# Optimization experiments

Measured on AMD Instinct MI355X. Metric: run time of the kernel, lower is better.

The kernel has to match this reference:

```python
import jax, jax.numpy as jnp
import numpy as np
from jax import lax
from jax.scipy.special import erf

EPS = 1e-5
B = 256

def _conv(x, w, stride):
    return lax.conv_general_dilated(x, w, (stride, stride), ((1, 1), (1, 1)),
                                    dimension_numbers=('NCHW', 'OIHW', 'NCHW'))

def lr_conv(x, alpha, betta, bias, stride):
    # Ternary weight distribution (LR-nets): p0 = P(w=0), p1 = P(w=1)
    p0 = jax.nn.sigmoid(alpha)
    p1 = (1.0 - p0) * jax.nn.sigmoid(betta)
    w_mean = 2.0 * p1 + p0 - 1.0          # E[w] = p1 - p_{-1}
    w_var = (1.0 - p0) - w_mean * w_mean  # Var[w] = E[w^2] - E[w]^2
    m = _conv(x, w_mean, stride) + bias[None, :, None, None]
    v = _conv(x * x, w_var, stride)
    return m, v

def sign_prob(m, v):
    # expected sign under CLT Gaussian: 2*Phi(m/sqrt(v)) - 1 = erf(m / sqrt(2 v))
    return erf(m / jnp.sqrt(2.0 * (v + EPS)))

def setup_inputs() -> dict:
    key = jax.random.key(0)
    ks = jax.random.split(key, 32)
    def n(k, shape, s=1.0):
        return jax.random.normal(k, shape, dtype=jnp.float32) * s
    inp = {}
    inp['x'] = n(ks[0], (B, 3, 32, 32))
    shapes = [(128, 3), (128, 128), (256, 128), (256, 256), (512, 256), (512, 512)]
    i = 1
    for li, (co, ci) in enumerate(shapes, start=1):
        inp['a%d' % li] = n(ks[i], (co, ci, 3, 3)); i += 1
        inp['b%d' % li] = n(ks[i], (co, ci, 3, 3)); i += 1
        inp['c%d' % li] = jnp.zeros((co,), jnp.float32)
    inp['bn_gamma'] = jnp.ones((512,), jnp.float32)
    inp['bn_beta'] = jnp.zeros((512,), jnp.float32)
    inp['fc1_w'] = n(ks[20], (1024, 8192), 0.01)
    inp['fc1_b'] = jnp.zeros((1024,), jnp.float32)
    inp['fc2_w'] = n(ks[21], (10, 1024), 0.03)
    inp['fc2_b'] = jnp.zeros((10,), jnp.float32)
    inp['noise6'] = n(ks[22], (B, 512, 4, 4))
    return inp

def reference(x, a1, b1, c1, a2, b2, c2, a3, b3, c3, a4, b4, c4, a5, b5, c5,
              a6, b6, c6, bn_gamma, bn_beta, fc1_w, fc1_b, fc2_w, fc2_b, noise6):
    h = x
    for (a, bt, c, s) in [(a1, b1, c1, 1), (a2, b2, c2, 2), (a3, b3, c3, 1),
                          (a4, b4, c4, 2), (a5, b5, c5, 1)]:
        m, v = lr_conv(h, a, bt, c, s)
        h = sign_prob(m, v)
    m, v = lr_conv(h, a6, b6, c6, 2)          # output_sample=True layer
    z = m + jnp.sqrt(v + EPS) * noise6        # reparameterized Gaussian sample
    mu = jnp.mean(z, axis=(0, 2, 3), keepdims=True)
    var = jnp.var(z, axis=(0, 2, 3), keepdims=True)
    z = bn_gamma[None, :, None, None] * (z - mu) / jnp.sqrt(var + EPS) + bn_beta[None, :, None, None]
    z = jax.nn.relu(z).reshape(z.shape[0], -1)  # [B, 8192]
    z = jax.nn.relu(z @ fc1_w.T + fc1_b)
    return z @ fc2_w.T + fc2_b
```

## Files before the change

kernel.cpp:

```cpp
#include <hip/hip_runtime.h>
#include <hip/hip_bf16.h>
#include <math.h>

#define EPS 1e-5f

typedef __hip_bfloat16 bf16;
typedef short s16x8 __attribute__((ext_vector_type(8)));
typedef float f32x4 __attribute__((ext_vector_type(4)));

constexpr int ilog2c(int v) { return v <= 1 ? 0 : 1 + ilog2c(v >> 1); }

__device__ __forceinline__ float ldin(const void* p, size_t i, int isbf) {
    return isbf ? __bfloat162float(((const bf16*)p)[i]) : ((const float*)p)[i];
}
__device__ __forceinline__ float b2f_bits(short s) {
    unsigned u = ((unsigned)(unsigned short)s) << 16;
    return __builtin_bit_cast(float, u);
}
__device__ __forceinline__ unsigned sqpk1(unsigned w) {
    float lo = __builtin_bit_cast(float, w << 16);
    float hi = __builtin_bit_cast(float, w & 0xffff0000u);
    lo *= lo; hi *= hi;
    unsigned ul = __builtin_bit_cast(unsigned, lo) + 0x8000u;
    unsigned uh = __builtin_bit_cast(unsigned, hi) + 0x8000u;
    return __builtin_amdgcn_perm(uh, ul, 0x07060302);
}
__device__ __forceinline__ uint4 sqpk4(uint4 u) {
    uint4 r;
    r.x = sqpk1(u.x); r.y = sqpk1(u.y); r.z = sqpk1(u.z); r.w = sqpk1(u.w);
    return r;
}

__device__ __forceinline__ void dma16(const void* g, void* l) {
    __builtin_amdgcn_global_load_lds(
        (const __attribute__((address_space(1))) void*)g,
        (__attribute__((address_space(3))) void*)l, 16, 0, 0);
}

__global__ __launch_bounds__(64) void detect_kernel(const void* __restrict__ x,
                                                    int* __restrict__ flags,
                                                    char* __restrict__ gA,
                                                    char* __restrict__ gB) {
    const unsigned* w = (const unsigned*)x;
    unsigned word = w[threadIdx.x];
    int e = (word >> 23) & 0xFF;
    bool ok = (word == 0u) || (e >= 0x70 && e <= 0x8E);
    unsigned long long m = __ballot(ok);
    if (threadIdx.x == 0) flags[0] = (__popcll(m) >= 32) ? 0 : 1;
    if (threadIdx.x < 16) ((uint4*)gA)[threadIdx.x] = (uint4){0, 0, 0, 0};
    else if (threadIdx.x < 32) ((uint4*)gB)[threadIdx.x - 16] = (uint4){0, 0, 0, 0};
}

__global__ __launch_bounds__(256) void prep_w_l1(
    const void* __restrict__ alpha, const void* __restrict__ betta,
    const int* __restrict__ flags, float* __restrict__ wmv, int n)
{
    int i = blockIdx.x * 256 + threadIdx.x;
    if (i >= n) return;
    int fl = flags[0];
    float a = ldin(alpha, i, fl), b = ldin(betta, i, fl);
    float p0 = 1.f / (1.f + expf(-a));
    float p1 = (1.f - p0) / (1.f + expf(-b));
    float m = 2.f * p1 + p0 - 1.f;
    wmv[i] = m;
    wmv[n + i] = (1.f - p0) - m * m;
}

__global__ __launch_bounds__(256) void prep_w_r(
    const void* __restrict__ alpha, const void* __restrict__ betta,
    const int* __restrict__ flags, bf16* __restrict__ wmr, bf16* __restrict__ wvr,
    int lc, int n)
{
    int o = blockIdx.x * 256 + threadIdx.x;
    if (o >= n) return;
    int fl = flags[0];
    int cotap = o >> lc;
    int ci = o & ((1 << lc) - 1);
    int co = cotap / 9;
    int tap = cotap - co * 9;
    int i = (((co << lc) + ci) * 9) + tap;
    float a = ldin(alpha, i, fl), b = ldin(betta, i, fl);
    float p0 = 1.f / (1.f + expf(-a));
    float p1 = (1.f - p0) / (1.f + expf(-b));
    float m = 2.f * p1 + p0 - 1.f;
    float v = (1.f - p0) - m * m;
    wmr[o] = __float2bfloat16(m);
    wvr[o] = __float2bfloat16(v);
}

__global__ __launch_bounds__(256) void permute_fc1(
    const void* __restrict__ w, const int* __restrict__ flags, bf16* __restrict__ wp)
{
    __shared__ float L[8192];
    const int fl = flags[0];
    int tid = threadIdx.x;
    int o = blockIdx.x;
    size_t srow = (size_t)o * 8192;
    for (int c = tid; c < 512; c += 256) {
        float v[16];
        if (fl) {
            const uint4* s = (const uint4*)((const bf16*)w + srow + c * 16);
            uint4 u0 = s[0], u1 = s[1];
            const unsigned short* h0 = (const unsigned short*)&u0;
            const unsigned short* h1 = (const unsigned short*)&u1;
#pragma unroll
            for (int j = 0; j < 8; j++) { v[j] = b2f_bits((short)h0[j]); v[8 + j] = b2f_bits((short)h1[j]); }
        } else {
            const float4* s = (const float4*)((const float*)w + srow + c * 16);
#pragma unroll
            for (int j = 0; j < 4; j++) {
                float4 t4 = s[j];
                v[j * 4 + 0] = t4.x; v[j * 4 + 1] = t4.y; v[j * 4 + 2] = t4.z; v[j * 4 + 3] = t4.w;
            }
        }
#pragma unroll
        for (int hw = 0; hw < 16; hw++) L[hw * 512 + c] = v[hw];
    }
    __syncthreads();
    for (int j = 0; j < 32; j++) {
        int idx = j * 256 + tid;
        wp[srow + idx] = __float2bfloat16(L[idx]);
    }
}

__global__ __launch_bounds__(256) void l1_conv(
    const void* __restrict__ x, const float* __restrict__ wmv,
    const void* __restrict__ bias, const int* __restrict__ flags,
    bf16* __restrict__ out)
{
    __shared__ float Xs[64][28];
    const int fl = flags[0];
    int tid = threadIdx.x;
    int pos0 = blockIdx.x * 64;
    int b = pos0 >> 10;
    for (int u = tid; u < 576; u += 256) {
        int p = u / 9, r = u - p * 9;
        int ci = r / 3, kh = r - ci * 3;
        int pos = pos0 + p;
        int oh = (pos >> 5) & 31, ow = pos & 31;
        int ih = oh - 1 + kh;
        bool okh = (unsigned)ih < 32u;
        size_t base = ((size_t)(b * 3 + ci) * 32 + ih) * 32;
#pragma unroll
        for (int kw = 0; kw < 3; kw++) {
            int iw = ow - 1 + kw;
            float v = (okh && (unsigned)iw < 32u) ? ldin(x, base + iw, fl) : 0.f;
            Xs[p][ci * 9 + kh * 3 + kw] = v;
        }
    }
    int c = tid & 127, pg = tid >> 7;
    float wm[27], wv[27];
#pragma unroll
    for (int k = 0; k < 27; k++) {
        wm[k] = wmv[c * 27 + k];
        wv[k] = wmv[3456 + c * 27 + k];
    }
    float bs = ldin(bias, c, fl);
    __syncthreads();
    for (int it = 0; it < 32; it++) {
        int p = it * 2 + pg;
        float aM = 0.f, aV = 0.f;
#pragma unroll
        for (int k = 0; k < 27; k++) {
            float xv = Xs[p][k];
            aM = fmaf(xv, wm[k], aM);
            aV = fmaf(xv * xv, wv[k], aV);
        }
        out[(size_t)(pos0 + p) * 128 + c] =
            __float2bfloat16(erff((aM + bs) * rsqrtf(2.f * (aV + EPS))));
    }
}

template<int CI, int CO, int H, int W, int S, int OH, int OW, int ACT, int COT>
__global__ __launch_bounds__(256, 3) void conv_gemm(
    const char* __restrict__ xreg,
    int zpoff,
    const bf16* __restrict__ wmr,
    const bf16* __restrict__ wvr,
    const void* __restrict__ bias, const void* __restrict__ noise,
    const int* __restrict__ flags, void* __restrict__ outp)
{
    constexpr int OHW = OH * OW;
    constexpr int KC = CI / 32;
    constexpr int NC = 9 * KC;
    constexpr int NW = COT / 16;
    constexpr int XB = 128 * 64;
    constexpr int WB = COT * 64;
    constexpr int BUFB = XB + 2 * WB;
    constexpr int LOHW = ilog2c(OHW), LOW = ilog2c(OW);
    static_assert((NC & 1) == 0 && COT == 64, "");

    __shared__ __align__(16) char smem[2 * BUFB];

    const int tid = threadIdx.x;
    const int lane = tid & 63, wv_ = tid >> 6;
    const int q = lane >> 4, l15 = lane & 15;
    const int pw = wv_ * 32;
    const int c0 = blockIdx.y * COT;
    const int bx128 = blockIdx.x * 128;

    const int sl   = (lane & 7) ^ (lane >> 3);
    const int row2 = 2 * (lane >> 3) + (sl >> 2);
    const int u16b = (sl & 3) * 16;

    int xb[4], ohS[4], owS[4];
#pragma unroll
    for (int kk = 0; kk < 4; kk++) {
        int P = bx128 + 16 * ((wv_ & 1) * 4 + kk) + row2;
        int bi = P >> LOHW;
        ohS[kk] = ((P >> LOW) & (OH - 1)) * S - 1;
        owS[kk] = (P & (OW - 1)) * S - 1;
        xb[kk] = bi * (H * W * CI * 2);
    }
    const char* wsb = (const char*)((wv_ == 3) ? wvr : wmr)
                      + (size_t)(c0 + row2) * (9 * CI * 2) + u16b;
    const int wdoff = XB + ((wv_ == 3) ? WB : 0);

    const int lA = (l15 >> 1) * 128 + (((((l15 & 1) << 2) | q) ^ (l15 >> 1)) << 4);
    const int abase = pw * 64 + lA;
    const int bbase = lA;

    f32x4 accM[2][4], accV[2][4];
#pragma unroll
    for (int i = 0; i < 2; i++)
#pragma unroll
        for (int j = 0; j < 4; j++) {
            accM[i][j] = (f32x4){0.f, 0.f, 0.f, 0.f};
            accV[i][j] = (f32x4){0.f, 0.f, 0.f, 0.f};
        }

    auto stage = [&](int t, int nb) {
        char* buf = smem + nb * BUFB;
        if (wv_ < 2) {
            const int tap = t / KC, kci = (t - tap * KC) * 64;
            const int kh = tap / 3, kw2 = tap - 3 * kh;
#pragma unroll
            for (int kk = 0; kk < 4; kk++) {
                int ih = ohS[kk] + kh, iw = owS[kk] + kw2;
                bool ok = ((unsigned)ih < (unsigned)H) && ((unsigned)iw < (unsigned)W);
                int off = xb[kk] + (ih * W + iw) * (CI * 2) + kci + u16b;
                off = ok ? off : zpoff;
                dma16(xreg + off, buf + ((wv_ & 1) * 4 + kk) * 1024);
            }
        } else {
            const char* s = wsb + t * 64;
            char* d = buf + wdoff;
#pragma unroll
            for (int k = 0; k < NW; k++)
                dma16(s + (size_t)k * (16 * 9 * CI * 2), d + k * 1024);
        }
    };

    auto compute = [&](int nb) {
        const char* buf = smem + nb * BUFB;
        s16x8 a[2], aq[2];
#pragma unroll
        for (int i = 0; i < 2; i++) {
            a[i] = *(const s16x8*)(buf + abase + i * 1024);
            uint4 uq = sqpk4(*(const uint4*)&a[i]);
            aq[i] = *(const s16x8*)&uq;
        }
#pragma unroll
        for (int j = 0; j < 4; j++) {
            s16x8 bm = *(const s16x8*)(buf + XB + bbase + j * 1024);
            s16x8 bv = *(const s16x8*)(buf + XB + WB + bbase + j * 1024);
#pragma unroll
            for (int i = 0; i < 2; i++) {
                accM[i][j] = __builtin_amdgcn_mfma_f32_16x16x32_bf16(a[i],  bm, accM[i][j], 0, 0, 0);
                accV[i][j] = __builtin_amdgcn_mfma_f32_16x16x32_bf16(aq[i], bv, accV[i][j], 0, 0, 0);
            }
        }
    };

#define BAR() asm volatile("s_waitcnt vmcnt(0) lgkmcnt(0)\n\ts_barrier" ::: "memory")

    stage(0, 0);
    for (int t = 0; t < NC; t += 2) {
        BAR();
        if (t + 1 < NC) stage(t + 1, 1);
        compute(0);
        BAR();
        if (t + 2 < NC) stage(t + 2, 0);
        compute(1);
    }
#undef BAR

    __syncthreads();
    const int fl = flags[0];
    if constexpr (ACT == 0) {
        bf16* Lact = (bf16*)smem;
        constexpr int LCB = ilog2c(COT * 2);
#pragma unroll
        for (int j = 0; j < 4; j++) {
            int co = c0 + j * 16 + l15;
            float bs = ldin(bias, co, fl);
#pragma unroll
            for (int i = 0; i < 2; i++) {
#pragma unroll
                for (int r = 0; r < 4; r++) {
                    int PPl = pw + i * 16 + q * 4 + r;
                    float mm = accM[i][j][r] + bs, vv = accV[i][j][r];
                    Lact[PPl * COT + j * 16 + l15] =
                        __float2bfloat16(erff(mm * rsqrtf(2.f * (vv + EPS))));
                }
            }
        }
        __syncthreads();
        constexpr int NST = (128 * COT * 2) / 4096;
#pragma unroll
        for (int k = 0; k < NST; k++) {
            int f = k * 4096 + tid * 16;
            int rowl = f >> LCB;
            int colb = f & ((COT * 2) - 1);
            uint4 va = *(const uint4*)((char*)smem + f);
            size_t gb = ((size_t)(bx128 + rowl) * CO + c0) * 2 + colb;
            *(uint4*)((char*)outp + gb) = va;
        }
    } else {
#pragma unroll
        for (int j = 0; j < 4; j++) {
            int co = c0 + j * 16 + l15;
            float bs = ldin(bias, co, fl);
#pragma unroll
            for (int i = 0; i < 2; i++) {
#pragma unroll
                for (int r = 0; r < 4; r++) {
                    int PP = bx128 + pw + i * 16 + q * 4 + r;
                    float mm = accM[i][j][r] + bs, vv = accV[i][j][r];
                    int bb = PP / OHW, hw = PP % OHW;
                    float nz = ldin(noise, ((size_t)bb * CO + co) * OHW + hw, fl);
                    ((float*)outp)[(size_t)PP * CO + co] = mm + sqrtf(vv + EPS) * nz;
                }
            }
        }
    }
}

__global__ __launch_bounds__(256) void fc1_gemm_sk(
    const bf16* __restrict__ A, const bf16* __restrict__ Wp,
    float* __restrict__ part)
{
    __shared__ bf16 Xs[128 * 40];
    __shared__ bf16 Ws[128 * 40];
    int tid = threadIdx.x;
    int lane = tid & 63, wv_ = tid >> 6;
    int q = lane >> 4, l15 = lane & 15;
    const int pw = (wv_ >> 1) * 64, cw = (wv_ & 1) * 64;
    const int p0 = blockIdx.x * 128, c0 = blockIdx.y * 128;
    const int kb = blockIdx.z * 1024;
    const int row_i = tid >> 1, half = tid & 1;

    f32x4 acc[4][4];
#pragma unroll
    for (int i = 0; i < 4; i++)
#pragma unroll
        for (int j = 0; j < 4; j++) acc[i][j] = (f32x4){0.f, 0.f, 0.f, 0.f};

    for (int k0 = kb; k0 < kb + 1024; k0 += 32) {
        __syncthreads();
        {
            const uint4* s = (const uint4*)(A + (size_t)(p0 + row_i) * 8192 + k0 + half * 16);
            uint4* d = (uint4*)(Xs + row_i * 40 + half * 16);
            d[0] = s[0]; d[1] = s[1];
        }
        {
            const uint4* s = (const uint4*)(Wp + (size_t)(c0 + row_i) * 8192 + k0 + half * 16);
            uint4* d = (uint4*)(Ws + row_i * 40 + half * 16);
            d[0] = s[0]; d[1] = s[1];
        }
        __syncthreads();
        s16x8 a[4], bb[4];
#pragma unroll
        for (int i = 0; i < 4; i++) {
            a[i]  = *(const s16x8*)(Xs + (pw + i * 16 + l15) * 40 + q * 8);
            bb[i] = *(const s16x8*)(Ws + (cw + i * 16 + l15) * 40 + q * 8);
        }
#pragma unroll
        for (int i = 0; i < 4; i++)
#pragma unroll
            for (int j = 0; j < 4; j++)
                acc[i][j] = __builtin_amdgcn_mfma_f32_16x16x32_bf16(a[i], bb[j], acc[i][j], 0, 0, 0);
    }

    float* pbase = part + (size_t)blockIdx.z * 256 * 1024;
#pragma unroll
    for (int j = 0; j < 4; j++) {
        int co = c0 + cw + j * 16 + l15;
#pragma unroll
        for (int i = 0; i < 4; i++) {
            f32x4 m4 = acc[i][j];
#pragma unroll
            for (int r = 0; r < 4; r++) {
                int P = p0 + pw + i * 16 + q * 4 + r;
                pbase[(size_t)P * 1024 + co] = m4[r];
            }
        }
    }
}

__global__ __launch_bounds__(256) void fc1_reduce(
    const float* __restrict__ part, const void* __restrict__ bias,
    const int* __restrict__ flags, float* __restrict__ out)
{
    int i = blockIdx.x * 256 + threadIdx.x;
    float s = 0.f;
#pragma unroll
    for (int k = 0; k < 8; k++) s += part[(size_t)k * 262144 + i];
    out[i] = fmaxf(s + ldin(bias, i & 1023, flags[0]), 0.f);
}

__global__ __launch_bounds__(256) void bn_part(const float* __restrict__ z,
                                               float4* __restrict__ partial)
{
    int blk = blockIdx.x;
    int t = threadIdx.x;
    float s0 = 0, ss0 = 0, s1 = 0, ss1 = 0;
    for (int p = 0; p < 32; p++) {
        float2 v = ((const float2*)z)[((size_t)(blk * 32 + p)) * 256 + t];
        s0 += v.x; ss0 += v.x * v.x;
        s1 += v.y; ss1 += v.y * v.y;
    }
    partial[blk * 256 + t] = make_float4(s0, ss0, s1, ss1);
}

__global__ __launch_bounds__(512) void bn_fin(
    const float4* __restrict__ partial, const void* __restrict__ gamma,
    const void* __restrict__ beta, const int* __restrict__ flags,
    float* __restrict__ sc, float* __restrict__ sh)
{
    int c = threadIdx.x;
    float s = 0, ss = 0;
    for (int j = 0; j < 128; j++) {
        float4 pv = partial[j * 256 + (c >> 1)];
        s += (c & 1) ? pv.z : pv.x;
        ss += (c & 1) ? pv.w : pv.y;
    }
    float mean = s * (1.f / 4096.f);
    float var = ss * (1.f / 4096.f) - mean * mean;
    int fl = flags[0];
    float scale = ldin(gamma, c, fl) * rsqrtf(var + EPS);
    sc[c] = scale;
    sh[c] = ldin(beta, c, fl) - mean * scale;
}

__global__ __launch_bounds__(256) void bn_apply(
    const float* __restrict__ z, const float* __restrict__ sc,
    const float* __restrict__ sh, bf16* __restrict__ zr)
{
    int i = blockIdx.x * 256 + threadIdx.x;
    int c = i & 511;
    float v = z[i] * sc[c] + sh[c];
    zr[i] = __float2bfloat16(fmaxf(v, 0.f));
}

__global__ __launch_bounds__(640) void fc2_kernel(
    const float* __restrict__ A, const void* __restrict__ W,
    const void* __restrict__ bias, const int* __restrict__ flags,
    void* __restrict__ out)
{
    const int fl = flags[0];
    int n = blockIdx.x;
    int o = threadIdx.x >> 6;
    int lane = threadIdx.x & 63;
    const float* a = A + (size_t)n * 1024;
    size_t wbase = (size_t)o * 1024;
    float s = 0.f;
    for (int i = lane; i < 1024; i += 64) s = fmaf(a[i], ldin(W, wbase + i, fl), s);
#pragma unroll
    for (int off = 32; off > 0; off >>= 1) s += __shfl_down(s, off);
    if (lane == 0) {
        float v = s + ldin(bias, o, fl);
        if (fl) ((bf16*)out)[n * 10 + o] = __float2bfloat16(v);
        else    ((float*)out)[n * 10 + o] = v;
    }
}

extern "C" void kernel_launch(void* const* d_in, const int* in_sizes, int n_in,
                              void* d_out, int out_size, void* d_ws, size_t ws_size,
                              hipStream_t stream)
{
    const void* x = d_in[0];
    const void *al[6], *be[6], *bi[6];
    for (int l = 0; l < 6; l++) {
        al[l] = d_in[1 + 3 * l];
        be[l] = d_in[2 + 3 * l];
        bi[l] = d_in[3 + 3 * l];
    }
    const void* bn_gamma = d_in[19];
    const void* bn_beta  = d_in[20];
    const void* fc1_w = d_in[21];
    const void* fc1_b = d_in[22];
    const void* fc2_w = d_in[23];
    const void* fc2_b = d_in[24];
    const void* noise = d_in[25];

    char* base = (char*)d_ws;
    size_t off = 0;
    auto alloc = [&](size_t bytes) { void* p = base + off; off += (bytes + 255) & ~(size_t)255; return p; };
    int* flags = (int*)alloc(256);
    float* w1 = (float*)alloc(2 * 3456 * sizeof(float));
    const int SwLC[5] = {7, 7, 8, 8, 9};
    const size_t Sw[5] = {147456, 294912, 589824, 1179648, 2359296};
    bf16 *wmr[5], *wvr[5];
    for (int l = 0; l < 5; l++) {
        wmr[l] = (bf16*)alloc(Sw[l] * sizeof(bf16));
        wvr[l] = (bf16*)alloc(Sw[l] * sizeof(bf16));
    }
    bf16* Wp   = (bf16*)alloc((size_t)1024 * 8192 * sizeof(bf16));
    float4* part = (float4*)alloc((size_t)128 * 256 * sizeof(float4));
    float* bnsc = (float*)alloc(512 * sizeof(float));
    float* bnsh = (float*)alloc(512 * sizeof(float));
    float* fc1o = (float*)alloc((size_t)256 * 1024 * sizeof(float));
    bf16* zr   = (bf16*)alloc((size_t)256 * 8192 * sizeof(bf16));

    const int ZPA = 67108864;
    const int ZPB = 16777216;
    char* RA = (char*)alloc((size_t)ZPA + 256);
    char* RB = (char*)alloc((size_t)ZPB + 256);
    float* z = (float*)RB;
    float* fc1part = (float*)(RB + 8388608);

    detect_kernel<<<1, 64, 0, stream>>>(x, flags, RA + ZPA, RB + ZPB);

    prep_w_l1<<<14, 256, 0, stream>>>(al[0], be[0], flags, w1, 3456);
    for (int l = 0; l < 5; l++) {
        int n = (int)Sw[l];
        prep_w_r<<<(n + 255) / 256, 256, 0, stream>>>(
            al[l + 1], be[l + 1], flags, wmr[l], wvr[l], SwLC[l], n);
    }
    permute_fc1<<<1024, 256, 0, stream>>>(fc1_w, flags, Wp);

    l1_conv<<<4096, 256, 0, stream>>>(x, w1, bi[0], flags, (bf16*)RA);

    conv_gemm<128, 128, 32, 32, 2, 16, 16, 0, 64><<<dim3(512, 2), 256, 0, stream>>>(
        RA, ZPA, wmr[0], wvr[0], bi[1], nullptr, flags, RB);
    conv_gemm<128, 256, 16, 16, 1, 16, 16, 0, 64><<<dim3(512, 4), 256, 0, stream>>>(
        RB, ZPB, wmr[1], wvr[1], bi[2], nullptr, flags, RA);
    conv_gemm<256, 256, 16, 16, 2, 8, 8, 0, 64><<<dim3(128, 4), 256, 0, stream>>>(
        RA, ZPA, wmr[2], wvr[2], bi[3], nullptr, flags, RB);
    conv_gemm<256, 512, 8, 8, 1, 8, 8, 0, 64><<<dim3(128, 8), 256, 0, stream>>>(
        RB, ZPB, wmr[3], wvr[3], bi[4], nullptr, flags, RA);
    conv_gemm<512, 512, 8, 8, 2, 4, 4, 1, 64><<<dim3(32, 8), 256, 0, stream>>>(
        RA, ZPA, wmr[4], wvr[4], bi[5], noise, flags, z);

    bn_part<<<128, 256, 0, stream>>>(z, part);
    bn_fin<<<1, 512, 0, stream>>>(part, bn_gamma, bn_beta, flags, bnsc, bnsh);
    bn_apply<<<8192, 256, 0, stream>>>(z, bnsc, bnsh, zr);

    fc1_gemm_sk<<<dim3(2, 8, 8), 256, 0, stream>>>(zr, Wp, fc1part);
    fc1_reduce<<<1024, 256, 0, stream>>>(fc1part, fc1_b, flags, fc1o);
    fc2_kernel<<<256, 640, 0, stream>>>(fc1o, fc2_w, fc2_b, flags, d_out);
}
```

Baseline: 709.1 us.

## Triple-buffer conv_gemm LDS pipeline with partial vmcnt waits and cached tap offsets

Moves the implicit-GEMM conv main loop from double to triple LDS buffering. Barriers now use `s_waitcnt vmcnt(4)`, so one stage's global-to-LDS DMA can stay in flight while the next buffer is computed, hiding more memory latency. Input address and bounds math is now recomputed only when the filter tap changes, with the channel-chunk offset added to cached offsets. Because of that, the zero-pad region must span a full channel row, so the zero block written by `detect_kernel` and the buffer padding are enlarged. The cost is 1.5x LDS per block, which could limit occupancy, and a stricter requirement that the chunk count be divisible by 3.

After: 723.0 us. About the same (+1.9%).

```diff
diff --git a/kernel.cpp b/kernel.cpp
--- a/kernel.cpp
+++ b/kernel.cpp
@@ -47,8 +47,12 @@
     bool ok = (word == 0u) || (e >= 0x70 && e <= 0x8E);
     unsigned long long m = __ballot(ok);
     if (threadIdx.x == 0) flags[0] = (__popcll(m) >= 32) ? 0 : 1;
-    if (threadIdx.x < 16) ((uint4*)gA)[threadIdx.x] = (uint4){0, 0, 0, 0};
-    else if (threadIdx.x < 32) ((uint4*)gB)[threadIdx.x - 16] = (uint4){0, 0, 0, 0};
+    uint4 z4 = (uint4){0, 0, 0, 0};
+#pragma unroll
+    for (int k = 0; k < 2; k++) {
+        ((uint4*)gA)[threadIdx.x * 2 + k] = z4;
+        ((uint4*)gB)[threadIdx.x * 2 + k] = z4;
+    }
 }
 
 __global__ __launch_bounds__(256) void prep_w_l1(
@@ -182,15 +186,16 @@
 {
     constexpr int OHW = OH * OW;
     constexpr int KC = CI / 32;
+    constexpr int LKC = ilog2c(KC);
     constexpr int NC = 9 * KC;
     constexpr int NW = COT / 16;
     constexpr int XB = 128 * 64;
     constexpr int WB = COT * 64;
     constexpr int BUFB = XB + 2 * WB;
     constexpr int LOHW = ilog2c(OHW), LOW = ilog2c(OW);
-    static_assert((NC & 1) == 0 && COT == 64, "");
-
-    __shared__ __align__(16) char smem[2 * BUFB];
+    static_assert(NC % 3 == 0 && COT == 64, "");
+
+    __shared__ __align__(16) char smem[3 * BUFB];
 
     const int tid = threadIdx.x;
     const int lane = tid & 63, wv_ = tid >> 6;
@@ -229,19 +234,27 @@
             accV[i][j] = (f32x4){0.f, 0.f, 0.f, 0.f};
         }
 
-    auto stage = [&](int t, int nb) {
-        char* buf = smem + nb * BUFB;
+    int curTap = -1;
+    int xoffs[4];
+
+    auto stage = [&](int t, char* buf) {
         if (wv_ < 2) {
-            const int tap = t / KC, kci = (t - tap * KC) * 64;
-            const int kh = tap / 3, kw2 = tap - 3 * kh;
-#pragma unroll
-            for (int kk = 0; kk < 4; kk++) {
-                int ih = ohS[kk] + kh, iw = owS[kk] + kw2;
-                bool ok = ((unsigned)ih < (unsigned)H) && ((unsigned)iw < (unsigned)W);
-                int off = xb[kk] + (ih * W + iw) * (CI * 2) + kci + u16b;
-                off = ok ? off : zpoff;
-                dma16(xreg + off, buf + ((wv_ & 1) * 4 + kk) * 1024);
+            const int tap = t >> LKC;
+            if (tap != curTap) {
+                curTap = tap;
+                const int kh = tap / 3, kw2 = tap - 3 * kh;
+#pragma unroll
+                for (int kk = 0; kk < 4; kk++) {
+                    int ih = ohS[kk] + kh, iw = owS[kk] + kw2;
+                    bool ok = ((unsigned)ih < (unsigned)H) && ((unsigned)iw < (unsigned)W);
+                    int off = xb[kk] + (ih * W + iw) * (CI * 2) + u16b;
+                    xoffs[kk] = ok ? off : zpoff;
+                }
             }
+            const int kci = (t & (KC - 1)) * 64;
+#pragma unroll
+            for (int kk = 0; kk < 4; kk++)
+                dma16(xreg + xoffs[kk] + kci, buf + ((wv_ & 1) * 4 + kk) * 1024);
         } else {
             const char* s = wsb + t * 64;
             char* d = buf + wdoff;
@@ -251,8 +264,7 @@
         }
     };
 
-    auto compute = [&](int nb) {
-        const char* buf = smem + nb * BUFB;
+    auto compute = [&](const char* buf) {
         s16x8 a[2], aq[2];
 #pragma unroll
         for (int i = 0; i < 2; i++) {
@@ -272,18 +284,28 @@
         }
     };
 
-#define BAR() asm volatile("s_waitcnt vmcnt(0) lgkmcnt(0)\n\ts_barrier" ::: "memory")
-
-    stage(0, 0);
-    for (int t = 0; t < NC; t += 2) {
-        BAR();
-        if (t + 1 < NC) stage(t + 1, 1);
-        compute(0);
-        BAR();
-        if (t + 2 < NC) stage(t + 2, 0);
-        compute(1);
-    }
-#undef BAR
+#define WAITBAR4() asm volatile("s_waitcnt vmcnt(4) lgkmcnt(0)\n\ts_barrier" ::: "memory")
+#define WAITBAR0() asm volatile("s_waitcnt vmcnt(0) lgkmcnt(0)\n\ts_barrier" ::: "memory")
+
+    char* const b0 = smem;
+    char* const b1 = smem + BUFB;
+    char* const b2 = smem + 2 * BUFB;
+
+    stage(0, b0);
+    stage(1, b1);
+    for (int t = 0; t < NC; t += 3) {
+        WAITBAR4();
+        stage(t + 2, b2);
+        compute(b0);
+        WAITBAR4();
+        if (t + 3 < NC) stage(t + 3, b0);
+        compute(b1);
+        if (t + 6 <= NC) { WAITBAR4(); } else { WAITBAR0(); }
+        if (t + 4 < NC) stage(t + 4, b1);
+        compute(b2);
+    }
+#undef WAITBAR4
+#undef WAITBAR0
 
     __syncthreads();
     const int fl = flags[0];
@@ -515,8 +537,8 @@
 
     const int ZPA = 67108864;
     const int ZPB = 16777216;
-    char* RA = (char*)alloc((size_t)ZPA + 256);
-    char* RB = (char*)alloc((size_t)ZPB + 256);
+    char* RA = (char*)alloc((size_t)ZPA + 2048);
+    char* RB = (char*)alloc((size_t)ZPB + 2048);
     float* z = (float*)RB;
     float* fc1part = (float*)(RB + 8388608);
 
```
